# Optimization experiments

Measured on AMD Instinct MI355X. Metric: run time of the kernel, lower is better.

The kernel has to match this reference:

```python
import jax, jax.numpy as jnp
import numpy as np

N = 50000   # nodes per domain graph
E = 800000  # edges per graph (avg degree 16)
IN = 512    # in_feats
H = 256     # n_hidden
C = 10      # n_classes
ALPHA = 1.0


def setup_inputs() -> dict:
    key = jax.random.key(0)
    ks = jax.random.split(key, 16)
    inp = {
        "features_s": jax.random.normal(ks[0], (N, IN), jnp.float32),
        "labels_s": jax.random.randint(ks[1], (N,), 0, C, jnp.int32),
        "features_t": jax.random.normal(ks[2], (N, IN), jnp.float32),
        "src_s": jax.random.randint(ks[3], (E,), 0, N, jnp.int32),
        "dst_s": jax.random.randint(ks[4], (E,), 0, N, jnp.int32),
        "src_t": jax.random.randint(ks[5], (E,), 0, N, jnp.int32),
        "dst_t": jax.random.randint(ks[6], (E,), 0, N, jnp.int32),
        # GraphConv layer 0: in_feats -> n_hidden (glorot-ish init)
        "W0": jax.random.normal(ks[7], (IN, H), jnp.float32) / np.float32(np.sqrt(IN)),
        "b0": jnp.zeros((H,), jnp.float32),
        # GraphConv layer 1: n_hidden -> n_hidden
        "W1": jax.random.normal(ks[8], (H, H), jnp.float32) / np.float32(np.sqrt(H)),
        "b1": jnp.zeros((H,), jnp.float32),
        # fc head: n_hidden -> n_classes
        "Wfc": jax.random.normal(ks[9], (H, C), jnp.float32) / np.float32(np.sqrt(H)),
        "bfc": jnp.zeros((C,), jnp.float32),
        # JS discriminator: (n_hidden*n_layers + n_classes) -> 2
        "Wd": jax.random.normal(ks[10], (H * 2 + C, 2), jnp.float32) / np.float32(np.sqrt(H * 2 + C)),
        "bd": jnp.zeros((2,), jnp.float32),
    }
    return inp


def _gconv(x, src, dst, W, b, n):
    # DGL GraphConv with norm='both': out = D_in^{-1/2} A D_out^{-1/2} x W + b, then relu.
    ones = jnp.ones(src.shape, x.dtype)
    deg_out = jax.ops.segment_sum(ones, src, num_segments=n)
    deg_in = jax.ops.segment_sum(ones, dst, num_segments=n)
    norm_src = jnp.maximum(deg_out, 1.0) ** -0.5   # [n]
    norm_dst = jnp.maximum(deg_in, 1.0) ** -0.5    # [n]
    h = (x * norm_src[:, None]) @ W                # [n, out] (mult-first: row scaling commutes)
    agg = jax.ops.segment_sum(h[src], dst, num_segments=n)  # gather-scatter SpMM
    return jax.nn.relu(agg * norm_dst[:, None] + b)


def reference(features_s, labels_s, features_t, src_s, dst_s, src_t, dst_t,
              W0, b0, W1, b1, Wfc, bfc, Wd, bd):
    # dropout omitted (eval-mode determinism)
    hs, ht = features_s, features_t
    s_list, t_list = [], []
    for (W, b) in ((W0, b0), (W1, b1)):
        hs = _gconv(hs, src_s, dst_s, W, b, N)
        ht = _gconv(ht, src_t, dst_t, W, b, N)
        s_list.append(hs)
        t_list.append(ht)
    logits_s = hs @ Wfc + bfc
    logits_t = ht @ Wfc + bfc
    s_list.append(logits_s)
    t_list.append(logits_t)

    # class loss: nll over log_softmax
    logp = jax.nn.log_softmax(logits_s, axis=-1)
    class_loss = -jnp.mean(jnp.take_along_axis(logp, labels_s[:, None].astype(jnp.int32), axis=1))

    # JS domain loss with gradient-reversal (identity in forward)
    s_f = jnp.concatenate(s_list, axis=1)  # [N, 2H+C]
    t_f = jnp.concatenate(t_list, axis=1)
    both = jnp.concatenate([s_f, t_f], axis=0)  # [2N, 2H+C]
    rev = -ALPHA * both + jax.lax.stop_gradient((1.0 + ALPHA) * both)  # GRL trick
    dlogits = rev @ Wd + bd
    dlogp = jax.nn.log_softmax(dlogits, axis=-1)
    dlabels = jnp.concatenate([jnp.zeros((N,), jnp.int32), jnp.ones((N,), jnp.int32)])
    domain_loss = -jnp.mean(jnp.take_along_axis(dlogp, dlabels[:, None], axis=1))

    return class_loss + 0.01 * domain_loss
```

## Files before the change

kernel.cpp:

```cpp
#include <hip/hip_runtime.h>
#include <cstdint>
#include <cstddef>

#define NN 50000
#define NNP 50016
#define EE 800000
#define INF 512
#define HH  256
#define CC  10
#define NB2 391
#define NTB 782
#define GB64 782
#define SPMM_BLOCKS 1600
#define HBIN 6250
#define HRNG 8
#define HSUB 32
#define SCAP 1536
#define ZROW NN

using bfrag = __attribute__((ext_vector_type(8))) __bf16;
using f32x4 = __attribute__((ext_vector_type(4))) float;

__device__ inline unsigned short f2bf(float x) {
    unsigned u = __builtin_bit_cast(unsigned, x);
    unsigned r = u + 0x7FFFu + ((u >> 16) & 1u);
    return (unsigned short)(r >> 16);
}
__device__ inline float bf2f(unsigned short h) {
    return __builtin_bit_cast(float, (unsigned)h << 16);
}

__device__ inline void gload_lds16(const void* gsrc, void* ldst) {
    __builtin_amdgcn_global_load_lds(
        (const __attribute__((address_space(1))) void*)gsrc,
        (__attribute__((address_space(3))) void*)ldst, 16, 0, 0);
}

template<int K>
__global__ void k_cast_wt(const float* __restrict__ W, ushort* __restrict__ Wt) {
    int idx = blockIdx.x * blockDim.x + threadIdx.x;
    if (idx >= K * HH) return;
    int n = idx / K, k = idx % K;
    Wt[idx] = f2bf(W[(size_t)k * HH + n]);
}

__global__ void k_cast_wtail(const float* __restrict__ Wfc, const float* __restrict__ Wd,
                             ushort* __restrict__ Wt1) {
    int idx = blockIdx.x * blockDim.x + threadIdx.x;
    if (idx >= 16 * HH) return;
    int n = idx >> 8, k = idx & 255;
    float v = 0.f;
    if (n < 10)       v = Wfc[(size_t)k * 10 + n];
    else if (n < 12)  v = Wd[(size_t)(HH + k) * 2 + (n - 10)];
    Wt1[idx] = f2bf(v);
}

__global__ void k_cast_wtail2(const float* __restrict__ Wd, ushort* __restrict__ Wt2) {
    int idx = blockIdx.x * blockDim.x + threadIdx.x;
    if (idx >= 16 * HH) return;
    int n = idx >> 8, k = idx & 255;
    float v = (n < 2) ? Wd[(size_t)k * 2 + n] : 0.f;
    Wt2[idx] = f2bf(v);
}

__global__ __launch_bounds__(256) void k_deghist(
        const int* __restrict__ src_s, const int* __restrict__ dst_s,
        const int* __restrict__ src_t, const int* __restrict__ dst_t,
        ushort* __restrict__ pcnt) {
    __shared__ int hist[HBIN];
    const int task = blockIdx.x >> 5;
    const int sub  = blockIdx.x & 31;
    const int arr = task >> 3, range = task & 7;
    const int* p = (arr == 0) ? src_s : (arr == 1) ? dst_s : (arr == 2) ? src_t : dst_t;
    const int4* p4 = reinterpret_cast<const int4*>(p);
    const int lo = range * HBIN;
    for (int j = threadIdx.x; j < HBIN; j += 256) hist[j] = 0;
    __syncthreads();
    for (int i = sub * 256 + (int)threadIdx.x; i < EE / 4; i += HSUB * 256) {
        int4 v = p4[i];
        int a0 = v.x - lo, a1 = v.y - lo, a2 = v.z - lo, a3 = v.w - lo;
        if ((unsigned)a0 < (unsigned)HBIN) atomicAdd(&hist[a0], 1);
        if ((unsigned)a1 < (unsigned)HBIN) atomicAdd(&hist[a1], 1);
        if ((unsigned)a2 < (unsigned)HBIN) atomicAdd(&hist[a2], 1);
        if ((unsigned)a3 < (unsigned)HBIN) atomicAdd(&hist[a3], 1);
    }
    __syncthreads();
    ushort* out = pcnt + ((size_t)task * HSUB + sub) * HBIN;
    for (int j = threadIdx.x; j < HBIN; j += 256) out[j] = (ushort)hist[j];
}

__global__ void k_degsum(const ushort* __restrict__ pcnt, int* __restrict__ cnt) {
    int g = blockIdx.x * blockDim.x + threadIdx.x;
    if (g >= 4 * NN) return;
    int arr = g / NN;
    int node = g - arr * NN;
    int range = node / HBIN;
    int j = node - range * HBIN;
    const ushort* p = pcnt + ((size_t)(arr * HRNG + range) * HSUB) * HBIN + j;
    int s = 0;
    #pragma unroll
    for (int k = 0; k < HSUB; ++k) s += p[(size_t)k * HBIN];
    cnt[g] = s;
}

__global__ void k_scan_blk(const int* __restrict__ cnt, int* __restrict__ off,
                           int* __restrict__ btot) {
    __shared__ int wsum[4];
    int tid = threadIdx.x, lane = tid & 63, wid = tid >> 6;
    int i = blockIdx.x * 256 + tid;
    int v = 0;
    if (i < 2 * NN) v = (i < NN) ? cnt[NN + i] : cnt[2 * NN + i];
    int s = v;
    #pragma unroll
    for (int o = 1; o < 64; o <<= 1) {
        int t = __shfl_up(s, o, 64);
        if (lane >= o) s += t;
    }
    if (lane == 63) wsum[wid] = s;
    __syncthreads();
    if (tid == 0) {
        int a = 0;
        #pragma unroll
        for (int w2 = 0; w2 < 4; ++w2) { int t = wsum[w2]; wsum[w2] = a; a += t; }
        btot[blockIdx.x] = a;
    }
    __syncthreads();
    if (i < 2 * NN) off[i] = wsum[wid] + s - v;
}

__global__ void k_scan_tops(const int* __restrict__ btot, int* __restrict__ bbase,
                            int* __restrict__ off) {
    __shared__ int wsum[8];
    int tid = threadIdx.x, lane = tid & 63, wid = tid >> 6;
    int v = (tid < NB2) ? btot[tid] : 0;
    int s = v;
    #pragma unroll
    for (int o = 1; o < 64; o <<= 1) {
        int t = __shfl_up(s, o, 64);
        if (lane >= o) s += t;
    }
    if (lane == 63) wsum[wid] = s;
    __syncthreads();
    if (tid == 0) {
        int a = 0;
        #pragma unroll
        for (int w2 = 0; w2 < 8; ++w2) { int t = wsum[w2]; wsum[w2] = a; a += t; }
        off[2 * NN] = a;
    }
    __syncthreads();
    if (tid < NB2) bbase[tid] = wsum[wid] + s - v;
}

__global__ void k_scan_fin(int* __restrict__ off, const int* __restrict__ bbase,
                           const int* __restrict__ cnt,
                           float* __restrict__ ns, float* __restrict__ nd,
                           ushort* __restrict__ y2) {
    if (blockIdx.x == 0) {
        #pragma unroll
        for (int j = 0; j < 2; ++j) {
            int idx = j * 256 + (int)threadIdx.x;
            int gg = idx >> 8, grp = (idx >> 5) & 7, c = idx & 31;
            y2[(((size_t)gg * 8 + grp) * NNP + ZROW) * 32 + c] = 0;
        }
    }
    int i = blockIdx.x * blockDim.x + threadIdx.x;
    if (i >= 2 * NN) return;
    int o = off[i] + bbase[i >> 8];
    off[i] = o;
    int co = (i < NN) ? cnt[i] : cnt[NN + i];
    int ci = (i < NN) ? cnt[NN + i] : cnt[2 * NN + i];
    ns[i] = 1.0f / sqrtf(fmaxf((float)co, 1.0f));
    nd[i] = 1.0f / sqrtf(fmaxf((float)ci, 1.0f));
}

__global__ void k_degpos(const ushort* __restrict__ pcnt, const int* __restrict__ off,
                         int* __restrict__ base2) {
    int i = blockIdx.x * blockDim.x + threadIdx.x;
    if (i >= 2 * NN) return;
    int g = (i < NN) ? 0 : 1;
    int node = i - g * NN;
    int range = node / HBIN;
    int bin = node - range * HBIN;
    int arr = g ? 3 : 1;
    const ushort* p = pcnt + ((size_t)(arr * HRNG + range) * HSUB) * HBIN + bin;
    int* b = base2 + ((size_t)(g * HRNG + range) * HSUB) * HBIN + bin;
    int run = off[i];
    #pragma unroll
    for (int s = 0; s < HSUB; ++s) {
        b[(size_t)s * HBIN] = run;
        run += p[(size_t)s * HBIN];
    }
}

__global__ __launch_bounds__(256) void k_fill3(
        const int* __restrict__ src_s, const int* __restrict__ dst_s,
        const int* __restrict__ src_t, const int* __restrict__ dst_t,
        const int* __restrict__ base2, int* __restrict__ csr_src) {
    __shared__ int cur[HBIN];
    const int combo = blockIdx.x & 15;
    const int sub = blockIdx.x >> 4;
    const int g = combo >> 3, range = combo & 7;
    const int4* d4 = reinterpret_cast<const int4*>(g ? dst_t : dst_s);
    const int4* s4 = reinterpret_cast<const int4*>(g ? src_t : src_s);
    const int lo = range * HBIN;
    const int* b = base2 + (size_t)combo * HSUB * HBIN + (size_t)sub * HBIN;
    for (int j = threadIdx.x; j < HBIN; j += 256) cur[j] = b[j];
    __syncthreads();
    for (int i = sub * 256 + (int)threadIdx.x; i < EE / 4; i += HSUB * 256) {
        int4 d = d4[i];
        int b0 = d.x - lo, b1 = d.y - lo, b2 = d.z - lo, b3 = d.w - lo;
        bool o0 = (unsigned)b0 < (unsigned)HBIN;
        bool o1 = (unsigned)b1 < (unsigned)HBIN;
        bool o2 = (unsigned)b2 < (unsigned)HBIN;
        bool o3 = (unsigned)b3 < (unsigned)HBIN;
        if (o0 | o1 | o2 | o3) {
            int4 s = s4[i];
            if (o0) csr_src[atomicAdd(&cur[b0], 1)] = s.x;
            if (o1) csr_src[atomicAdd(&cur[b1], 1)] = s.y;
            if (o2) csr_src[atomicAdd(&cur[b2], 1)] = s.z;
            if (o3) csr_src[atomicAdd(&cur[b3], 1)] = s.w;
        }
    }
}

template<int K, bool F32A>
__global__ __launch_bounds__(256, 4) void k_gemm2(
        const void* __restrict__ Ap_s, const void* __restrict__ Ap_t,
        const ushort* __restrict__ Bt, const float* __restrict__ ns2,
        ushort* __restrict__ y2) {
    __shared__ ushort As[64 * 64];
    __shared__ ushort Bs[256 * 64];
    const int g = blockIdx.x >= GB64 ? 1 : 0;
    const void* Ap = g ? Ap_t : Ap_s;
    const float* ns = ns2 + (size_t)g * NN;
    ushort* y2g = y2 + (size_t)g * 8 * NNP * 32;
    const int m0 = (blockIdx.x - g * GB64) * 64;
    const int t = threadIdx.x;
    const int wid = t >> 6, lane = t & 63;
    const int wc = wid * 64;
    const int l15 = lane & 15, lg = lane >> 4;

    f32x4 acc[4][4];
    #pragma unroll
    for (int m = 0; m < 4; ++m)
        #pragma unroll
        for (int n = 0; n < 4; ++n)
            acc[m][n] = {0.f, 0.f, 0.f, 0.f};

    const int srow = t >> 3;
    const int schunk = t & 7;

    for (int k0 = 0; k0 < K; k0 += 64) {
        if constexpr (F32A) {
            #pragma unroll
            for (int i = 0; i < 2; ++i) {
                int row = srow + i * 32;
                int sw = ((schunk ^ (row & 7)) * 8);
                int m = m0 + row; if (m >= NN) m = NN - 1;
                const float* ap = (const float*)Ap + (size_t)m * K + k0 + schunk * 8;
                float4 f0 = *reinterpret_cast<const float4*>(ap);
                float4 f1 = *reinterpret_cast<const float4*>(ap + 4);
                uint4 va;
                va.x = (unsigned)f2bf(f0.x) | ((unsigned)f2bf(f0.y) << 16);
                va.y = (unsigned)f2bf(f0.z) | ((unsigned)f2bf(f0.w) << 16);
                va.z = (unsigned)f2bf(f1.x) | ((unsigned)f2bf(f1.y) << 16);
                va.w = (unsigned)f2bf(f1.z) | ((unsigned)f2bf(f1.w) << 16);
                *reinterpret_cast<uint4*>(&As[row * 64 + sw]) = va;
            }
        } else {
            #pragma unroll
            for (int i = 0; i < 2; ++i) {
                int row = srow + i * 32;
                int sw = ((schunk ^ (row & 7)) * 8);
                int m = m0 + row; if (m >= NN) m = NN - 1;
                const ushort* gsrc = (const ushort*)Ap + (size_t)m * K + k0 + sw;
                gload_lds16(gsrc, &As[(size_t)(wid * 8 + i * 32) * 64]);
            }
        }
        #pragma unroll
        for (int i = 0; i < 8; ++i) {
            int row = srow + i * 32;
            int sw = ((schunk ^ (row & 7)) * 8);
            const ushort* gsrc = &Bt[(size_t)row * K + k0 + sw];
            gload_lds16(gsrc, &Bs[(size_t)(wid * 8 + i * 32) * 64]);
        }
        __syncthreads();
        #pragma unroll
        for (int kk = 0; kk < 64; kk += 32) {
            const int kc = kk >> 3;
            bfrag af[4];
            #pragma unroll
            for (int m = 0; m < 4; ++m) {
                int row = m * 16 + l15;
                af[m] = *reinterpret_cast<const bfrag*>(&As[row * 64 + (((lg + kc) ^ (row & 7)) * 8)]);
            }
            #pragma unroll
            for (int n = 0; n < 4; ++n) {
                int row = wc + n * 16 + l15;
                bfrag bg = *reinterpret_cast<const bfrag*>(&Bs[row * 64 + (((lg + kc) ^ (row & 7)) * 8)]);
                #pragma unroll
                for (int m = 0; m < 4; ++m)
                    acc[m][n] = __builtin_amdgcn_mfma_f32_16x16x32_bf16(af[m], bg, acc[m][n], 0, 0, 0);
            }
        }
        __syncthreads();
    }

    ushort* tile = Bs;
    #pragma unroll
    for (int m = 0; m < 4; ++m) {
        #pragma unroll
        for (int r = 0; r < 4; ++r) {
            int rloc = m * 16 + lg * 4 + r;
            int rowg = m0 + rloc;
            float nsv = ns[rowg < NN ? rowg : NN - 1];
            #pragma unroll
            for (int n = 0; n < 4; ++n)
                tile[rloc * 256 + wc + n * 16 + l15] = f2bf(acc[m][n][r] * nsv);
        }
    }
    __syncthreads();
    {
        int row = t >> 2, sub = t & 3;
        int m = m0 + row;
        if (m < NN) {
            #pragma unroll
            for (int grp = 0; grp < 8; ++grp) {
                uint4 v = *reinterpret_cast<const uint4*>(&tile[row * 256 + grp * 32 + sub * 8]);
                *reinterpret_cast<uint4*>(&y2g[((size_t)grp * NNP + m) * 32 + sub * 8]) = v;
            }
        }
    }
}

__device__ inline void add8(float* a, uint4 v) {
    a[0] += __builtin_bit_cast(float, v.x << 16);
    a[1] += __builtin_bit_cast(float, v.x & 0xffff0000u);
    a[2] += __builtin_bit_cast(float, v.y << 16);
    a[3] += __builtin_bit_cast(float, v.y & 0xffff0000u);
    a[4] += __builtin_bit_cast(float, v.z << 16);
    a[5] += __builtin_bit_cast(float, v.z & 0xffff0000u);
    a[6] += __builtin_bit_cast(float, v.w << 16);
    a[7] += __builtin_bit_cast(float, v.w & 0xffff0000u);
}

__global__ __launch_bounds__(256) void k_spmm6(
        const ushort* __restrict__ y2, const int* __restrict__ off,
        const int* __restrict__ csr_src, const float* __restrict__ nd_arr,
        const float* __restrict__ bias, ushort* __restrict__ h_out) {
    __shared__ int sidx[4][SCAP];
    const int grp = blockIdx.x & 7;
    const int blk = blockIdx.x >> 3;
    const int tid = threadIdx.x;
    const int lane = tid & 63, wid = tid >> 6;
    const int slot = lane >> 2;
    const int sub = lane & 3;
    const ushort* ybase = y2 + (size_t)grp * NNP * 32 + sub * 8;

    const int nb = (blk * 4 + wid) * 64;
    int s_wave0 = 0, cnt = 0;
    if (nb < NN) {
        int nend = nb + 64 < NN ? nb + 64 : NN;
        s_wave0 = off[nb];
        cnt = off[nend] - s_wave0;
    }
    int stage = cnt < SCAP ? cnt : SCAP;
    for (int j = lane; j < stage; j += 64)
        sidx[wid][j] = csr_src[s_wave0 + j];
    __syncthreads();

    float bia[8];
    #pragma unroll
    for (int j = 0; j < 8; ++j) bia[j] = bias[grp * 32 + sub * 8 + j];

    int e0[4], e1[4];
    float a[4][8];
    #pragma unroll
    for (int c = 0; c < 4; ++c) {
        int n = nb + c * 16 + slot;
        bool v = n < NN;
        e0[c] = v ? off[n] - s_wave0 : 0;
        e1[c] = v ? off[n + 1] - s_wave0 : 0;
        #pragma unroll
        for (int j = 0; j < 8; ++j) a[c][j] = 0.f;
    }
    int tmax = max(max(e1[0] - e0[0], e1[1] - e0[1]), max(e1[2] - e0[2], e1[3] - e0[3]));

    if (cnt <= SCAP) {
        for (int t = 0; t < tmax; t += 2) {
            uint4 v[8];
            #pragma unroll
            for (int u = 0; u < 2; ++u)
                #pragma unroll
                for (int c = 0; c < 4; ++c) {
                    int ec = e0[c] + t + u;
                    bool val = ec < e1[c];
                    int ecc = val ? ec : 0;
                    int id = sidx[wid][ecc];
                    id = val ? id : ZROW;
                    v[u * 4 + c] = *reinterpret_cast<const uint4*>(&ybase[(size_t)id * 32]);
                }
            #pragma unroll
            for (int u = 0; u < 2; ++u)
                #pragma unroll
                for (int c = 0; c < 4; ++c) add8(a[c], v[u * 4 + c]);
        }
    } else {
        for (int t = 0; t < tmax; t += 2) {
            uint4 v[8];
            #pragma unroll
            for (int u = 0; u < 2; ++u)
                #pragma unroll
                for (int c = 0; c < 4; ++c) {
                    int ec = e0[c] + t + u;
                    bool val = ec < e1[c];
                    int ecc = val ? ec : 0;
                    int id = csr_src[s_wave0 + ecc];
                    id = val ? id : ZROW;
                    v[u * 4 + c] = *reinterpret_cast<const uint4*>(&ybase[(size_t)id * 32]);
                }
            #pragma unroll
            for (int u = 0; u < 2; ++u)
                #pragma unroll
                for (int c = 0; c < 4; ++c) add8(a[c], v[u * 4 + c]);
        }
    }

    #pragma unroll
    for (int c = 0; c < 4; ++c) {
        int n = nb + c * 16 + slot;
        if (n >= NN) continue;
        float nd = nd_arr[n];
        ushort r[8];
        #pragma unroll
        for (int j = 0; j < 8; ++j) r[j] = f2bf(fmaxf(a[c][j] * nd + bia[j], 0.f));
        uint4 pk;
        pk.x = (unsigned)r[0] | ((unsigned)r[1] << 16);
        pk.y = (unsigned)r[2] | ((unsigned)r[3] << 16);
        pk.z = (unsigned)r[4] | ((unsigned)r[5] << 16);
        pk.w = (unsigned)r[6] | ((unsigned)r[7] << 16);
        *reinterpret_cast<uint4*>(&h_out[(size_t)n * 256 + grp * 32 + sub * 8]) = pk;
    }
}

__global__ __launch_bounds__(256) void k_tail_mfma(
        const ushort* __restrict__ h0s, const ushort* __restrict__ h0t,
        const ushort* __restrict__ h1s, const ushort* __restrict__ h1t,
        const ushort* __restrict__ Wt1, const ushort* __restrict__ Wt2,
        const float* __restrict__ bfc, const float* __restrict__ bd,
        const int* __restrict__ labels,
        float* __restrict__ pcls, float* __restrict__ pdom) {
    __shared__ float sT1[4][16][17];
    __shared__ float sT2[4][16][17];
    __shared__ float sc[4], sd[4];
    const int g = blockIdx.x >= NTB ? 1 : 0;
    const int bi = blockIdx.x - g * NTB;
    const ushort* h0 = g ? h0t : h0s;
    const ushort* h1 = g ? h1t : h1s;
    const int tid = threadIdx.x;
    const int wid = tid >> 6, lane = tid & 63;
    const int l15 = lane & 15, lg = lane >> 4;
    const int base = bi * 64 + wid * 16;

    int arow = base + l15; if (arow >= NN) arow = NN - 1;
    const ushort* a1 = h1 + (size_t)arow * 256 + lg * 8;
    const ushort* a0 = h0 + (size_t)arow * 256 + lg * 8;
    const ushort* b1 = Wt1 + (size_t)l15 * 256 + lg * 8;
    const ushort* b2 = Wt2 + (size_t)l15 * 256 + lg * 8;
    f32x4 acc1 = {0.f, 0.f, 0.f, 0.f};
    f32x4 acc2 = {0.f, 0.f, 0.f, 0.f};
    #pragma unroll
    for (int kk = 0; kk < 8; ++kk) {
        bfrag af1 = *reinterpret_cast<const bfrag*>(a1 + kk * 32);
        bfrag bg1 = *reinterpret_cast<const bfrag*>(b1 + kk * 32);
        acc1 = __builtin_amdgcn_mfma_f32_16x16x32_bf16(af1, bg1, acc1, 0, 0, 0);
        bfrag af0 = *reinterpret_cast<const bfrag*>(a0 + kk * 32);
        bfrag bg2 = *reinterpret_cast<const bfrag*>(b2 + kk * 32);
        acc2 = __builtin_amdgcn_mfma_f32_16x16x32_bf16(af0, bg2, acc2, 0, 0, 0);
    }
    #pragma unroll
    for (int j = 0; j < 4; ++j) {
        sT1[wid][lg * 4 + j][l15] = acc1[j];
        sT2[wid][lg * 4 + j][l15] = acc2[j];
    }
    __syncthreads();

    float cls = 0.f, dom = 0.f;
    int n = base + lane;
    if (lane < 16 && n < NN) {
        float lgt[10];
        #pragma unroll
        for (int c = 0; c < 10; ++c) lgt[c] = sT1[wid][lane][c] + bfc[c];
        float dl0 = bd[0] + sT2[wid][lane][0] + sT1[wid][lane][10];
        float dl1 = bd[1] + sT2[wid][lane][1] + sT1[wid][lane][11];
        if (g == 0) {
            float m = lgt[0];
            #pragma unroll
            for (int c = 1; c < 10; ++c) m = fmaxf(m, lgt[c]);
            float s = 0.f;
            #pragma unroll
            for (int c = 0; c < 10; ++c) s += expf(lgt[c] - m);
            int lab = labels[n];
            float tgt = lgt[0];
            #pragma unroll
            for (int c = 1; c < 10; ++c) tgt = (c == lab) ? lgt[c] : tgt;
            cls = -(tgt - (m + logf(s)));
        }
        float m2 = fmaxf(dl0, dl1);
        float lse2 = m2 + logf(expf(dl0 - m2) + expf(dl1 - m2));
        dom = -((g ? dl1 : dl0) - lse2);
    }
    #pragma unroll
    for (int o = 1; o < 16; o <<= 1) {
        cls += __shfl_xor(cls, o, 64);
        dom += __shfl_xor(dom, o, 64);
    }
    if (lane == 0) { sc[wid] = cls; sd[wid] = dom; }
    __syncthreads();
    if (tid == 0) {
        float c = sc[0] + sc[1] + sc[2] + sc[3];
        float d = sd[0] + sd[1] + sd[2] + sd[3];
        if (g == 0) pcls[bi] = c;
        pdom[g * NTB + bi] = d;
    }
}

__global__ void k_finalize(const float* __restrict__ pcls, const float* __restrict__ pdom,
                           float* __restrict__ out) {
    __shared__ float sc[4], sd[4];
    int tid = threadIdx.x, lane = tid & 63, wid = tid >> 6;
    float c = 0.f, d = 0.f;
    for (int i = tid; i < NTB; i += 256) c += pcls[i];
    for (int i = tid; i < 2 * NTB; i += 256) d += pdom[i];
    #pragma unroll
    for (int o = 32; o; o >>= 1) {
        c += __shfl_xor(c, o, 64);
        d += __shfl_xor(d, o, 64);
    }
    if (lane == 0) { sc[wid] = c; sd[wid] = d; }
    __syncthreads();
    if (tid == 0) {
        float ct = sc[0] + sc[1] + sc[2] + sc[3];
        float dt = sd[0] + sd[1] + sd[2] + sd[3];
        out[0] = ct / (float)NN + 0.01f * (dt / (float)(2 * NN));
    }
}

extern "C" void kernel_launch(void* const* d_in, const int* in_sizes, int n_in,
                              void* d_out, int out_size, void* d_ws, size_t ws_size,
                              hipStream_t stream) {
    const float* features_s = (const float*)d_in[0];
    const int*   labels_s   = (const int*)d_in[1];
    const float* features_t = (const float*)d_in[2];
    const int*   src_s      = (const int*)d_in[3];
    const int*   dst_s      = (const int*)d_in[4];
    const int*   src_t      = (const int*)d_in[5];
    const int*   dst_t      = (const int*)d_in[6];
    const float* W0         = (const float*)d_in[7];
    const float* b0         = (const float*)d_in[8];
    const float* W1         = (const float*)d_in[9];
    const float* b1         = (const float*)d_in[10];
    const float* Wfc        = (const float*)d_in[11];
    const float* bfc        = (const float*)d_in[12];
    const float* Wd         = (const float*)d_in[13];
    const float* bd         = (const float*)d_in[14];
    float* out = (float*)d_out;

    auto align256 = [](size_t x) { return (x + 255) & ~(size_t)255; };
    char* w = (char*)d_ws;
    ushort* h0s    = (ushort*)w; w += align256((size_t)NN * HH * 2);
    ushort* h0t    = (ushort*)w; w += align256((size_t)NN * HH * 2);
    ushort* h1s    = (ushort*)w; w += align256((size_t)NN * HH * 2);
    ushort* h1t    = (ushort*)w; w += align256((size_t)NN * HH * 2);
    ushort* y2     = (ushort*)w; w += align256((size_t)2 * 8 * NNP * 32 * 2);
    ushort* W0t    = (ushort*)w; w += align256((size_t)INF * HH * 2);
    ushort* W1t    = (ushort*)w; w += align256((size_t)HH * HH * 2);
    ushort* Wt1    = (ushort*)w; w += align256((size_t)16 * HH * 2);
    ushort* Wt2    = (ushort*)w; w += align256((size_t)16 * HH * 2);
    float* ns      = (float*)w;  w += align256((size_t)2 * NN * 4);
    float* nd      = (float*)w;  w += align256((size_t)2 * NN * 4);
    int*   cnt     = (int*)w;    w += align256((size_t)4 * NN * 4);
    int*   csr_off = (int*)w;    w += align256((size_t)(2 * NN + 1) * 4);
    int*   csr_src = (int*)w;    w += align256((size_t)2 * EE * 4);
    int*   btot    = (int*)w;    w += align256((size_t)NB2 * 4);
    int*   bbase   = (int*)w;    w += align256((size_t)NB2 * 4);
    float* pcls    = (float*)w;  w += align256((size_t)NTB * 4);
    float* pdom    = (float*)w;  w += align256((size_t)2 * NTB * 4);
    ushort* pcnt   = (ushort*)w; w += align256((size_t)4 * HRNG * HSUB * HBIN * 2);
    int*   base2   = (int*)w;    w += align256((size_t)2 * HRNG * HSUB * HBIN * 4);

    const int TB = 256;
    k_cast_wt<INF><<<(INF * HH + TB - 1) / TB, TB, 0, stream>>>(W0, W0t);
    k_cast_wt<HH><<<(HH * HH + TB - 1) / TB, TB, 0, stream>>>(W1, W1t);
    k_cast_wtail<<<(16 * HH + TB - 1) / TB, TB, 0, stream>>>(Wfc, Wd, Wt1);
    k_cast_wtail2<<<(16 * HH + TB - 1) / TB, TB, 0, stream>>>(Wd, Wt2);

    k_deghist<<<4 * HRNG * HSUB, TB, 0, stream>>>(src_s, dst_s, src_t, dst_t, pcnt);
    k_degsum<<<(4 * NN + TB - 1) / TB, TB, 0, stream>>>(pcnt, cnt);
    k_scan_blk<<<NB2, TB, 0, stream>>>(cnt, csr_off, btot);
    k_scan_tops<<<1, 512, 0, stream>>>(btot, bbase, csr_off);
    k_scan_fin<<<NB2, TB, 0, stream>>>(csr_off, bbase, cnt, ns, nd, y2);
    k_degpos<<<NB2, TB, 0, stream>>>(pcnt, csr_off, base2);
    k_fill3<<<16 * HSUB, TB, 0, stream>>>(src_s, dst_s, src_t, dst_t, base2, csr_src);

    const int* off_s = csr_off;
    const int* off_t = csr_off + NN;
    ushort* y2s = y2;
    ushort* y2t = y2 + (size_t)8 * NNP * 32;

    k_gemm2<INF, true><<<2 * GB64, TB, 0, stream>>>(features_s, features_t, W0t, ns, y2);
    k_spmm6<<<SPMM_BLOCKS, TB, 0, stream>>>(y2s, off_s, csr_src, nd, b0, h0s);
    k_spmm6<<<SPMM_BLOCKS, TB, 0, stream>>>(y2t, off_t, csr_src, nd + NN, b0, h0t);

    k_gemm2<HH, false><<<2 * GB64, TB, 0, stream>>>(h0s, h0t, W1t, ns, y2);
    k_spmm6<<<SPMM_BLOCKS, TB, 0, stream>>>(y2s, off_s, csr_src, nd, b1, h1s);
    k_spmm6<<<SPMM_BLOCKS, TB, 0, stream>>>(y2t, off_t, csr_src, nd + NN, b1, h1t);

    k_tail_mfma<<<2 * NTB, TB, 0, stream>>>(h0s, h0t, h1s, h1t, Wt1, Wt2, bfc, bd,
                                            labels_s, pcls, pdom);
    k_finalize<<<1, TB, 0, stream>>>(pcls, pdom, out);
}
```

Measured before the change: 433.2 us.

## Sort nodes by in-degree to balance SpMM wave work

Adds three kernels that build a counting-sort permutation of destination nodes by in-degree (capped at 63) for each graph. The SpMM kernel then assigns nodes to lanes in this degree-sorted order, so nodes handled together in a wave have similar edge counts and the loop over the per-wave maximum degree wastes fewer iterations. The LDS staging of source indices is dropped, because sorted nodes no longer have contiguous CSR ranges, so index loads now go to global memory. Output rows become scattered writes, and three small launches are added to setup.

```diff
diff --git a/kernel.cpp b/kernel.cpp
--- a/kernel.cpp
+++ b/kernel.cpp
@@ -15,7 +15,6 @@
 #define HBIN 6250
 #define HRNG 8
 #define HSUB 32
-#define SCAP 1536
 #define ZROW NN
 
 using bfrag = __attribute__((ext_vector_type(8))) __bf16;
@@ -220,6 +219,67 @@
             if (o2) csr_src[atomicAdd(&cur[b2], 1)] = s.z;
             if (o3) csr_src[atomicAdd(&cur[b3], 1)] = s.w;
         }
+    }
+}
+
+__global__ __launch_bounds__(256) void k_phist(const int* __restrict__ off,
+                                               ushort* __restrict__ phist) {
+    __shared__ int h[128];
+    int tid = threadIdx.x;
+    if (tid < 128) h[tid] = 0;
+    __syncthreads();
+    int i = blockIdx.x * 256 + tid;
+    if (i < 2 * NN) {
+        int d = off[i + 1] - off[i];
+        int g = (i < NN) ? 0 : 1;
+        int bin = g * 64 + (d < 63 ? d : 63);
+        atomicAdd(&h[bin], 1);
+    }
+    __syncthreads();
+    if (tid < 128) phist[(size_t)blockIdx.x * 128 + tid] = (ushort)h[tid];
+}
+
+__global__ void k_pscan(const ushort* __restrict__ phist, int* __restrict__ pbase) {
+    __shared__ int tbin[128];
+    int tid = threadIdx.x;
+    if (tid < 128) {
+        int tot = 0;
+        for (int b = 0; b < NB2; ++b) tot += phist[(size_t)b * 128 + tid];
+        tbin[tid] = tot;
+    }
+    __syncthreads();
+    if (tid < 2) {
+        int run = tid * NN;
+        for (int j = 0; j < 64; ++j) {
+            int t = tbin[tid * 64 + j];
+            tbin[tid * 64 + j] = run;
+            run += t;
+        }
+    }
+    __syncthreads();
+    if (tid < 128) {
+        int run = tbin[tid];
+        for (int b = 0; b < NB2; ++b) {
+            pbase[(size_t)b * 128 + tid] = run;
+            run += phist[(size_t)b * 128 + tid];
+        }
+    }
+}
+
+__global__ __launch_bounds__(256) void k_pscat(const int* __restrict__ off,
+                                               const int* __restrict__ pbase,
+                                               int* __restrict__ perm) {
+    __shared__ int cur[128];
+    int tid = threadIdx.x;
+    if (tid < 128) cur[tid] = pbase[(size_t)blockIdx.x * 128 + tid];
+    __syncthreads();
+    int i = blockIdx.x * 256 + tid;
+    if (i < 2 * NN) {
+        int d = off[i + 1] - off[i];
+        int g = (i < NN) ? 0 : 1;
+        int bin = g * 64 + (d < 63 ? d : 63);
+        int pos = atomicAdd(&cur[bin], 1);
+        perm[pos] = i - g * NN;
     }
 }
 
@@ -344,11 +404,11 @@
     a[7] += __builtin_bit_cast(float, v.w & 0xffff0000u);
 }
 
-__global__ __launch_bounds__(256) void k_spmm6(
+__global__ __launch_bounds__(256) void k_spmm7(
         const ushort* __restrict__ y2, const int* __restrict__ off,
-        const int* __restrict__ csr_src, const float* __restrict__ nd_arr,
-        const float* __restrict__ bias, ushort* __restrict__ h_out) {
-    __shared__ int sidx[4][SCAP];
+        const int* __restrict__ csr_src, const int* __restrict__ perm,
+        const float* __restrict__ nd_arr, const float* __restrict__ bias,
+        ushort* __restrict__ h_out) {
     const int grp = blockIdx.x & 7;
     const int blk = blockIdx.x >> 3;
     const int tid = threadIdx.x;
@@ -358,78 +418,49 @@
     const ushort* ybase = y2 + (size_t)grp * NNP * 32 + sub * 8;
 
     const int nb = (blk * 4 + wid) * 64;
-    int s_wave0 = 0, cnt = 0;
-    if (nb < NN) {
-        int nend = nb + 64 < NN ? nb + 64 : NN;
-        s_wave0 = off[nb];
-        cnt = off[nend] - s_wave0;
-    }
-    int stage = cnt < SCAP ? cnt : SCAP;
-    for (int j = lane; j < stage; j += 64)
-        sidx[wid][j] = csr_src[s_wave0 + j];
-    __syncthreads();
 
     float bia[8];
     #pragma unroll
     for (int j = 0; j < 8; ++j) bia[j] = bias[grp * 32 + sub * 8 + j];
 
-    int e0[4], e1[4];
+    int pn[4], e0[4], e1[4];
     float a[4][8];
     #pragma unroll
     for (int c = 0; c < 4; ++c) {
-        int n = nb + c * 16 + slot;
-        bool v = n < NN;
-        e0[c] = v ? off[n] - s_wave0 : 0;
-        e1[c] = v ? off[n + 1] - s_wave0 : 0;
+        int idx = nb + c * 16 + slot;
+        bool v = idx < NN;
+        pn[c] = v ? perm[idx] : 0;
+        e0[c] = off[pn[c]];
+        e1[c] = v ? off[pn[c] + 1] : e0[c];
         #pragma unroll
         for (int j = 0; j < 8; ++j) a[c][j] = 0.f;
     }
     int tmax = max(max(e1[0] - e0[0], e1[1] - e0[1]), max(e1[2] - e0[2], e1[3] - e0[3]));
 
-    if (cnt <= SCAP) {
-        for (int t = 0; t < tmax; t += 2) {
-            uint4 v[8];
-            #pragma unroll
-            for (int u = 0; u < 2; ++u)
-                #pragma unroll
-                for (int c = 0; c < 4; ++c) {
-                    int ec = e0[c] + t + u;
-                    bool val = ec < e1[c];
-                    int ecc = val ? ec : 0;
-                    int id = sidx[wid][ecc];
-                    id = val ? id : ZROW;
-                    v[u * 4 + c] = *reinterpret_cast<const uint4*>(&ybase[(size_t)id * 32]);
-                }
-            #pragma unroll
-            for (int u = 0; u < 2; ++u)
-                #pragma unroll
-                for (int c = 0; c < 4; ++c) add8(a[c], v[u * 4 + c]);
-        }
-    } else {
-        for (int t = 0; t < tmax; t += 2) {
-            uint4 v[8];
-            #pragma unroll
-            for (int u = 0; u < 2; ++u)
-                #pragma unroll
-                for (int c = 0; c < 4; ++c) {
-                    int ec = e0[c] + t + u;
-                    bool val = ec < e1[c];
-                    int ecc = val ? ec : 0;
-                    int id = csr_src[s_wave0 + ecc];
-                    id = val ? id : ZROW;
-                    v[u * 4 + c] = *reinterpret_cast<const uint4*>(&ybase[(size_t)id * 32]);
-                }
-            #pragma unroll
-            for (int u = 0; u < 2; ++u)
-                #pragma unroll
-                for (int c = 0; c < 4; ++c) add8(a[c], v[u * 4 + c]);
-        }
+    for (int t = 0; t < tmax; t += 2) {
+        uint4 v[8];
+        #pragma unroll
+        for (int u = 0; u < 2; ++u)
+            #pragma unroll
+            for (int c = 0; c < 4; ++c) {
+                int ec = e0[c] + t + u;
+                bool val = ec < e1[c];
+                int ecc = val ? ec : e0[c];
+                int id = csr_src[ecc];
+                id = val ? id : ZROW;
+                v[u * 4 + c] = *reinterpret_cast<const uint4*>(&ybase[(size_t)id * 32]);
+            }
+        #pragma unroll
+        for (int u = 0; u < 2; ++u)
+            #pragma unroll
+            for (int c = 0; c < 4; ++c) add8(a[c], v[u * 4 + c]);
     }
 
     #pragma unroll
     for (int c = 0; c < 4; ++c) {
-        int n = nb + c * 16 + slot;
-        if (n >= NN) continue;
+        int idx = nb + c * 16 + slot;
+        if (idx >= NN) continue;
+        int n = pn[c];
         float nd = nd_arr[n];
         ushort r[8];
         #pragma unroll
@@ -588,6 +619,9 @@
     float* pdom    = (float*)w;  w += align256((size_t)2 * NTB * 4);
     ushort* pcnt   = (ushort*)w; w += align256((size_t)4 * HRNG * HSUB * HBIN * 2);
     int*   base2   = (int*)w;    w += align256((size_t)2 * HRNG * HSUB * HBIN * 4);
+    ushort* phist  = (ushort*)w; w += align256((size_t)NB2 * 128 * 2);
+    int*   pbase   = (int*)w;    w += align256((size_t)NB2 * 128 * 4);
+    int*   perm    = (int*)w;    w += align256((size_t)2 * NN * 4);
 
     const int TB = 256;
     k_cast_wt<INF><<<(INF * HH + TB - 1) / TB, TB, 0, stream>>>(W0, W0t);
@@ -603,18 +637,22 @@
     k_degpos<<<NB2, TB, 0, stream>>>(pcnt, csr_off, base2);
     k_fill3<<<16 * HSUB, TB, 0, stream>>>(src_s, dst_s, src_t, dst_t, base2, csr_src);
 
+    k_phist<<<NB2, TB, 0, stream>>>(csr_off, phist);
+    k_pscan<<<1, TB, 0, stream>>>(phist, pbase);
+    k_pscat<<<NB2, TB, 0, stream>>>(csr_off, pbase, perm);
+
     const int* off_s = csr_off;
     const int* off_t = csr_off + NN;
     ushort* y2s = y2;
     ushort* y2t = y2 + (size_t)8 * NNP * 32;
 
     k_gemm2<INF, true><<<2 * GB64, TB, 0, stream>>>(features_s, features_t, W0t, ns, y2);
-    k_spmm6<<<SPMM_BLOCKS, TB, 0, stream>>>(y2s, off_s, csr_src, nd, b0, h0s);
-    k_spmm6<<<SPMM_BLOCKS, TB, 0, stream>>>(y2t, off_t, csr_src, nd + NN, b0, h0t);
+    k_spmm7<<<SPMM_BLOCKS, TB, 0, stream>>>(y2s, off_s, csr_src, perm, nd, b0, h0s);
+    k_spmm7<<<SPMM_BLOCKS, TB, 0, stream>>>(y2t, off_t, csr_src, perm + NN, nd + NN, b0, h0t);
 
     k_gemm2<HH, false><<<2 * GB64, TB, 0, stream>>>(h0s, h0t, W1t, ns, y2);
-    k_spmm6<<<SPMM_BLOCKS, TB, 0, stream>>>(y2s, off_s, csr_src, nd, b1, h1s);
-    k_spmm6<<<SPMM_BLOCKS, TB, 0, stream>>>(y2t, off_t, csr_src, nd + NN, b1, h1t);
+    k_spmm7<<<SPMM_BLOCKS, TB, 0, stream>>>(y2s, off_s, csr_src, perm, nd, b1, h1s);
+    k_spmm7<<<SPMM_BLOCKS, TB, 0, stream>>>(y2t, off_t, csr_src, perm + NN, nd + NN, b1, h1t);
 
     k_tail_mfma<<<2 * NTB, TB, 0, stream>>>(h0s, h0t, h1s, h1t, Wt1, Wt2, bfc, bd,
                                             labels_s, pcls, pdom);
```

Result: slower. 595.1 us (+37.4%).
